# Optimization experiments

Hardware: AMD Instinct MI355X
Metric: run time of the kernel (lower is better)

Reference implementation:

```python
import jax, jax.numpy as jnp
import numpy as np

EMBED, HEADS, LEVELS, POINTS = 256, 8, 4, 4
SPATIAL_SHAPES = np.array([[128, 128], [64, 64], [32, 32], [16, 16]], dtype=np.int32)


def _grid_init_bias():
    # Faithful reproduction of the sampling_offsets bias init (per-head directional grid).
    thetas = np.arange(HEADS, dtype=np.float32) * (2.0 * np.pi / HEADS)
    g = np.stack([np.cos(thetas), np.sin(thetas)], -1)
    g = g / np.abs(g).max(-1, keepdims=True)
    g = np.tile(g.reshape(HEADS, 1, 1, 2), (1, LEVELS, POINTS, 1))
    for i in range(POINTS):
        g[:, :, i, :] *= i + 1
    return g.reshape(-1).astype(np.float32)


def setup_inputs() -> dict:
    key = jax.random.key(0)
    ks = jax.random.split(key, 8)
    bs = 2
    V = int((SPATIAL_SHAPES[:, 0] * SPATIAL_SHAPES[:, 1]).sum())  # 21760
    Q = V  # encoder self-attention
    C = EMBED
    n_off = HEADS * LEVELS * POINTS * 2
    n_attn = HEADS * LEVELS * POINTS
    inv_sqrt_c = 1.0 / np.sqrt(C)
    return {
        "query": jax.random.normal(ks[0], (bs, Q, C), jnp.float32),
        "value": jax.random.normal(ks[1], (bs, V, C), jnp.float32),
        "reference_points": jax.random.uniform(ks[2], (bs, Q, LEVELS, 2), jnp.float32),
        "spatial_shapes": SPATIAL_SHAPES,  # static int array
        # learned parameters (torch Linear stored as [in, out]: y = x @ W + b)
        "W_off": jax.random.normal(ks[3], (C, n_off), jnp.float32) * 0.01,
        "b_off": jnp.asarray(_grid_init_bias()),
        "W_attn": jax.random.normal(ks[4], (C, n_attn), jnp.float32) * 0.02,
        "b_attn": jnp.zeros((n_attn,), jnp.float32),
        "W_v": jax.random.normal(ks[5], (C, C), jnp.float32) * inv_sqrt_c,
        "b_v": jnp.zeros((C,), jnp.float32),
        "W_out": jax.random.normal(ks[6], (C, C), jnp.float32) * inv_sqrt_c,
        "b_out": jnp.zeros((C,), jnp.float32),
    }


def _ms_deform_attn(query, value, reference_points, shapes,
                    W_off, b_off, W_attn, b_attn, W_v, b_v, W_out, b_out):
    bs, Q, C = query.shape
    d = C // HEADS
    # value projection -> [bs, heads, V, d]
    val = (value @ W_v + b_v).reshape(bs, -1, HEADS, d).transpose(0, 2, 1, 3)
    # sampling offsets and attention weights from query
    off = (query @ W_off + b_off).reshape(bs, Q, HEADS, LEVELS, POINTS, 2)
    attn = jax.nn.softmax(
        (query @ W_attn + b_attn).reshape(bs, Q, HEADS, LEVELS * POINTS), axis=-1
    ).reshape(bs, Q, HEADS, LEVELS, POINTS)
    # offset normalizer is (W, H) per level
    norm = jnp.asarray(np.stack([shapes[:, 1], shapes[:, 0]], -1), jnp.float32)  # [L,2]
    loc = reference_points[:, :, None, :, None, :] + off / norm[None, None, None, :, None, :]

    out = jnp.zeros((bs, HEADS, Q, d), query.dtype)
    start = 0
    for l in range(LEVELS):
        H, W = int(shapes[l, 0]), int(shapes[l, 1])
        v_l = val[:, :, start:start + H * W]  # [bs, heads, H*W, d]
        start += H * W
        loc_l = loc[:, :, :, l]    # [bs, Q, heads, P, 2] in [0,1]
        attn_l = attn[:, :, :, l]  # [bs, Q, heads, P]
        # grid_sample(align_corners=False, padding_mode='zeros') semantics
        g = 2.0 * loc_l - 1.0
        x = (g[..., 0] + 1.0) * 0.5 * W - 0.5
        y = (g[..., 1] + 1.0) * 0.5 * H - 0.5
        x0 = jnp.floor(x)
        y0 = jnp.floor(y)
        for dx in (0, 1):
            for dy in (0, 1):
                xi = x0 + dx
                yi = y0 + dy
                w = (1.0 - jnp.abs(x - xi)) * (1.0 - jnp.abs(y - yi))
                valid = (xi >= 0) & (xi <= W - 1) & (yi >= 0) & (yi <= H - 1)
                w = jnp.where(valid, w, 0.0) * attn_l  # fused corner + attention weight
                idx = (jnp.clip(yi, 0, H - 1).astype(jnp.int32) * W
                       + jnp.clip(xi, 0, W - 1).astype(jnp.int32))  # [bs,Q,heads,P]
                idx_t = jnp.transpose(idx, (0, 2, 1, 3)).reshape(bs, HEADS, Q * POINTS)
                vals = jnp.take_along_axis(v_l, idx_t[..., None], axis=2)
                vals = vals.reshape(bs, HEADS, Q, POINTS, d)
                out = out + jnp.einsum('bhqpd,bqhp->bhqd', vals, w)
    out = out.transpose(0, 2, 1, 3).reshape(bs, Q, C)  # heads-major channel layout
    return out @ W_out + b_out


def reference(query, value, reference_points, spatial_shapes,
              W_off, b_off, W_attn, b_attn, W_v, b_v, W_out, b_out):
    shapes = np.asarray(spatial_shapes)  # static
    return _ms_deform_attn(query, value, reference_points, shapes,
                           W_off, b_off, W_attn, b_attn, W_v, b_v, W_out, b_out)
```

## Files before the change

kernel.cpp:

```cpp
#include <hip/hip_runtime.h>
#include <math.h>

#define QN 21760
#define MTOT 43520
#define SZBQC 11141120

typedef __attribute__((ext_vector_type(8))) short bf16x8;
typedef __attribute__((ext_vector_type(4))) float f32x4;
typedef __attribute__((ext_vector_type(2))) float f32x2;

__device__ inline ushort f2bf(float f) {
  union { float f; uint u; } v; v.f = f;
  return (ushort)((v.u + 0x7FFFu + ((v.u >> 16) & 1u)) >> 16);
}
__device__ inline float bflo(uint u) { union { uint u; float f; } v; v.u = u << 16; return v.f; }
__device__ inline float bfhi(uint u) { union { uint u; float f; } v; v.u = u & 0xFFFF0000u; return v.f; }
__device__ inline uint pk2(float lo, float hi) { return (uint)f2bf(lo) | ((uint)f2bf(hi) << 16); }

__device__ inline void g2l(const ushort* g, ushort* l) {
  __builtin_amdgcn_global_load_lds(
      (const __attribute__((address_space(1))) void*)g,
      (__attribute__((address_space(3))) void*)l, 16, 0, 0);
}

__global__ __launch_bounds__(256) void prep_weights(
    const float* __restrict__ Wv, const float* __restrict__ Wout,
    const float* __restrict__ Woff, const float* __restrict__ Wattn,
    const float* __restrict__ boff, const float* __restrict__ battn,
    ushort* __restrict__ wv_t, ushort* __restrict__ wout_t,
    ushort* __restrict__ wol_t, float* __restrict__ biasf) {
  int bidx = blockIdx.x, t = threadIdx.x;
  if (bidx < 256) {
    int idx = bidx * 256 + t; int n = idx >> 8, k = idx & 255;
    wv_t[idx] = f2bf(Wv[(size_t)k * 256 + n]);
  } else if (bidx < 512) {
    int idx = (bidx - 256) * 256 + t; int n = idx >> 8, k = idx & 255;
    wout_t[idx] = f2bf(Wout[(size_t)k * 256 + n]);
  } else {
    int idx = (bidx - 512) * 256 + t; int n = idx >> 8, k = idx & 255;
    float v = (n < 256) ? Woff[(size_t)k * 256 + n] : Wattn[(size_t)k * 128 + (n - 256)];
    wol_t[idx] = f2bf(v);
    if (idx < 384) biasf[idx] = (idx < 256) ? boff[idx] : battn[idx - 256];
  }
}

__global__ __launch_bounds__(256) void cast2_bf16(
    const float* __restrict__ q, const float* __restrict__ v,
    ushort* __restrict__ qo, ushort* __restrict__ vo) {
  int i = blockIdx.x * 256 + threadIdx.x;
  const float* src; ushort* dst;
  if (i >= SZBQC / 8) { src = q; dst = qo; i -= SZBQC / 8; }
  else { src = v; dst = vo; }
  const float4* xp = (const float4*)src;
  float4 a = xp[2 * i], b = xp[2 * i + 1];
  uint4 o;
  o.x = pk2(a.x, a.y); o.y = pk2(a.z, a.w);
  o.z = pk2(b.x, b.y); o.w = pk2(b.z, b.w);
  ((uint4*)dst)[i] = o;
}


__global__ __launch_bounds__(256) void gemm_in(
    const ushort* __restrict__ vbf, const ushort* __restrict__ qbf,
    const ushort* __restrict__ Wv, const ushort* __restrict__ Wol,
    const float* __restrict__ bv, const float* __restrict__ bol,
    ushort* __restrict__ val_out, float* __restrict__ offlog) {
  __shared__ ushort As[2][4096];
  __shared__ ushort Bs[2][4096];
  const int t = threadIdx.x, wave = t >> 6, lane = t & 63;
  const int bx = blockIdx.x, bm = blockIdx.y * 128;
  const bool isVal = bx < 2;
  const ushort* A  = isVal ? vbf : qbf;
  const ushort* Bt = isVal ? (Wv + (size_t)bx * 128 * 256)
                           : (Wol + (size_t)(bx - 2) * 128 * 256);
  const int wm = (wave >> 1) * 64, wn = (wave & 1) * 64;
  const int l15 = lane & 15, l4 = lane >> 4;
  const int pc = l4 ^ ((l15 >> 1) & 3);

  const int srow = lane >> 2;
  const int sch  = (lane & 3) ^ ((lane >> 3) & 3);
  const ushort* Ag = A + (size_t)(bm + 32 * wave + srow) * 256 + sch * 8;
  const ushort* Bg = Bt + (size_t)(32 * wave + srow) * 256 + sch * 8;
  ushort* la[2] = { &As[0][(32 * wave) * 32], &As[1][(32 * wave) * 32] };
  ushort* lb[2] = { &Bs[0][(32 * wave) * 32], &Bs[1][(32 * wave) * 32] };

  f32x4 acc[4][4];
#pragma unroll
  for (int i = 0; i < 4; ++i)
#pragma unroll
    for (int j = 0; j < 4; ++j) acc[i][j] = (f32x4){0.f, 0.f, 0.f, 0.f};

  g2l(Ag, la[0]); g2l(Ag + 16 * 256, la[0] + 16 * 32);
  g2l(Bg, lb[0]); g2l(Bg + 16 * 256, lb[0] + 16 * 32);

  for (int k = 0; k < 8; ++k) {
    __syncthreads();
    const int cur = k & 1, nxt = cur ^ 1;
    if (k < 7) {
      int k1 = (k + 1) * 32;
      g2l(Ag + k1, la[nxt]); g2l(Ag + 16 * 256 + k1, la[nxt] + 16 * 32);
      g2l(Bg + k1, lb[nxt]); g2l(Bg + 16 * 256 + k1, lb[nxt] + 16 * 32);
    }
    bf16x8 af[4], bfr[4];
#pragma unroll
    for (int mi = 0; mi < 4; ++mi)
      af[mi] = *(const bf16x8*)&As[cur][(wm + mi * 16 + l15) * 32 + pc * 8];
#pragma unroll
    for (int ni = 0; ni < 4; ++ni)
      bfr[ni] = *(const bf16x8*)&Bs[cur][(wn + ni * 16 + l15) * 32 + pc * 8];
#pragma unroll
    for (int mi = 0; mi < 4; ++mi)
#pragma unroll
      for (int ni = 0; ni < 4; ++ni)
        acc[mi][ni] = __builtin_amdgcn_mfma_f32_16x16x32_bf16(af[mi], bfr[ni], acc[mi][ni], 0, 0, 0);
  }

  if (isVal) {
#pragma unroll
    for (int mi = 0; mi < 4; ++mi)
#pragma unroll
      for (int ni = 0; ni < 4; ++ni) {
        int col = bx * 128 + wn + ni * 16 + l15;
        float bb = bv[col];
        int hh = col >> 5, c = col & 31;
#pragma unroll
        for (int r = 0; r < 4; ++r) {
          int row = bm + wm + mi * 16 + l4 * 4 + r;
          int b = (row >= QN) ? 1 : 0;
          int vpos = row - b * QN;
          val_out[((size_t)(b * 8 + hh) * QN + vpos) * 32 + c] = f2bf(acc[mi][ni][r] + bb);
        }
      }
  } else {
#pragma unroll
    for (int mi = 0; mi < 4; ++mi)
#pragma unroll
      for (int ni = 0; ni < 4; ++ni) {
        int col = (bx - 2) * 128 + wn + ni * 16 + l15;
        float bb = bol[col];
#pragma unroll
        for (int r = 0; r < 4; ++r) {
          int row = bm + wm + mi * 16 + l4 * 4 + r;
          offlog[(size_t)row * 384 + col] = acc[mi][ni][r] + bb;
        }
      }
  }
}

__global__ __launch_bounds__(256) void gemm_out(
    const ushort* __restrict__ A, const ushort* __restrict__ Bt,
    const float* __restrict__ bias, float* __restrict__ C) {
  __shared__ ushort As[2][4096];
  __shared__ ushort Bs[2][4096];
  const int t = threadIdx.x, wave = t >> 6, lane = t & 63;
  const int bm = blockIdx.y * 128, bn = blockIdx.x * 128;
  const int wm = (wave >> 1) * 64, wn = (wave & 1) * 64;
  const int l15 = lane & 15, l4 = lane >> 4;
  const int pc = l4 ^ ((l15 >> 1) & 3);

  const int srow = lane >> 2;
  const int sch  = (lane & 3) ^ ((lane >> 3) & 3);
  const ushort* Ag = A + (size_t)(bm + 32 * wave + srow) * 256 + sch * 8;
  const ushort* Bg = Bt + (size_t)(bn + 32 * wave + srow) * 256 + sch * 8;
  ushort* la[2] = { &As[0][(32 * wave) * 32], &As[1][(32 * wave) * 32] };
  ushort* lb[2] = { &Bs[0][(32 * wave) * 32], &Bs[1][(32 * wave) * 32] };

  f32x4 acc[4][4];
#pragma unroll
  for (int i = 0; i < 4; ++i)
#pragma unroll
    for (int j = 0; j < 4; ++j) acc[i][j] = (f32x4){0.f, 0.f, 0.f, 0.f};

  g2l(Ag, la[0]); g2l(Ag + 16 * 256, la[0] + 16 * 32);
  g2l(Bg, lb[0]); g2l(Bg + 16 * 256, lb[0] + 16 * 32);

  for (int k = 0; k < 8; ++k) {
    __syncthreads();
    const int cur = k & 1, nxt = cur ^ 1;
    if (k < 7) {
      int k1 = (k + 1) * 32;
      g2l(Ag + k1, la[nxt]); g2l(Ag + 16 * 256 + k1, la[nxt] + 16 * 32);
      g2l(Bg + k1, lb[nxt]); g2l(Bg + 16 * 256 + k1, lb[nxt] + 16 * 32);
    }
    bf16x8 af[4], bfr[4];
#pragma unroll
    for (int mi = 0; mi < 4; ++mi)
      af[mi] = *(const bf16x8*)&As[cur][(wm + mi * 16 + l15) * 32 + pc * 8];
#pragma unroll
    for (int ni = 0; ni < 4; ++ni)
      bfr[ni] = *(const bf16x8*)&Bs[cur][(wn + ni * 16 + l15) * 32 + pc * 8];
#pragma unroll
    for (int mi = 0; mi < 4; ++mi)
#pragma unroll
      for (int ni = 0; ni < 4; ++ni)
        acc[mi][ni] = __builtin_amdgcn_mfma_f32_16x16x32_bf16(af[mi], bfr[ni], acc[mi][ni], 0, 0, 0);
  }

#pragma unroll
  for (int mi = 0; mi < 4; ++mi)
#pragma unroll
    for (int ni = 0; ni < 4; ++ni) {
      int col = bn + wn + ni * 16 + l15;
      float bb = bias[col];
#pragma unroll
      for (int r = 0; r < 4; ++r) {
        int row = bm + wm + mi * 16 + l4 * 4 + r;
        C[(size_t)row * 256 + col] = acc[mi][ni][r] + bb;
      }
    }
}

__device__ inline void fma8(f32x2* a, uint4 u, float wv) {
  f32x2 ww = { wv, wv }; f32x2 v;
  v.x = bflo(u.x); v.y = bfhi(u.x); a[0] += v * ww;
  v.x = bflo(u.y); v.y = bfhi(u.y); a[1] += v * ww;
  v.x = bflo(u.z); v.y = bfhi(u.z); a[2] += v * ww;
  v.x = bflo(u.w); v.y = bfhi(u.w); a[3] += v * ww;
}

__global__ __launch_bounds__(256) void msda_sample(
    const ushort* __restrict__ val, const float* __restrict__ offlog,
    const float* __restrict__ ref, ushort* __restrict__ interm) {
  const int lsz[4]    = {128, 64, 32, 16};
  const int lstart[4] = {0, 16384, 20480, 21504};

  int h   = blockIdx.x & 7;
  int z   = blockIdx.x >> 3;
  int sub = threadIdx.x & 3;
  int bq  = z * 64 + (threadIdx.x >> 2);
  int b   = (bq >= QN) ? 1 : 0;

  const float* lgp = offlog + (size_t)bq * 384 + 256 + h * 16;
  float w[16];
  {
    float4 a0 = *(const float4*)(lgp);
    float4 a1 = *(const float4*)(lgp + 4);
    float4 a2 = *(const float4*)(lgp + 8);
    float4 a3 = *(const float4*)(lgp + 12);
    w[0]=a0.x; w[1]=a0.y; w[2]=a0.z; w[3]=a0.w;
    w[4]=a1.x; w[5]=a1.y; w[6]=a1.z; w[7]=a1.w;
    w[8]=a2.x; w[9]=a2.y; w[10]=a2.z; w[11]=a2.w;
    w[12]=a3.x; w[13]=a3.y; w[14]=a3.z; w[15]=a3.w;
  }
  float m = -1e30f;
#pragma unroll
  for (int s = 0; s < 16; ++s) m = fmaxf(m, w[s]);
  float sum = 0.f;
#pragma unroll
  for (int s = 0; s < 16; ++s) { w[s] = __expf(w[s] - m); sum += w[s]; }
  float inv = 1.f / sum;

  const float* offp = offlog + (size_t)bq * 384 + h * 32;
  const float* refp = ref + (size_t)bq * 8;
  const ushort* vb  = val + ((size_t)(b * 8 + h) * QN) * 32 + sub * 8;

  f32x2 acc[4];
#pragma unroll
  for (int i = 0; i < 4; ++i) acc[i] = (f32x2){0.f, 0.f};

#pragma unroll
  for (int l = 0; l < 4; ++l) {
    float4 o0 = *(const float4*)(offp + l * 8);
    float4 o1 = *(const float4*)(offp + l * 8 + 4);
    float ox[4] = { o0.x, o0.z, o1.x, o1.z };
    float oy[4] = { o0.y, o0.w, o1.y, o1.w };
    const int   W = lsz[l];
    const float fW = (float)W;
    const int   base = lstart[l];
    const float rx = refp[l * 2 + 0], ry = refp[l * 2 + 1];
#pragma unroll
    for (int p = 0; p < 4; ++p) {
      float x = rx * fW + ox[p] - 0.5f;
      float y = ry * fW + oy[p] - 0.5f;
      float x0f = floorf(x), y0f = floorf(y);
      int   x0 = (int)x0f,   y0 = (int)y0f;
      float fx = x - x0f,    fy = y - y0f;
      float a = w[l * 4 + p] * inv;
      const ushort* r0 = vb + (size_t)(base + y0 * W + x0) * 32;
      const ushort* r1 = r0 + (size_t)W * 32;

      if (x0 >= 0 && y0 >= 0 && x0 + 1 < W && y0 + 1 < W) {
        uint4 u00 = *(const uint4*)r0;
        uint4 u10 = *(const uint4*)(r0 + 32);
        uint4 u01 = *(const uint4*)r1;
        uint4 u11 = *(const uint4*)(r1 + 32);
        float w00 = (1.f - fx) * (1.f - fy) * a;
        float w10 = fx * (1.f - fy) * a;
        float w01 = (1.f - fx) * fy * a;
        float w11 = fx * fy * a;
        fma8(acc, u00, w00); fma8(acc, u10, w10);
        fma8(acc, u01, w01); fma8(acc, u11, w11);
      } else {
        float wx0 = (x0 >= 0 && x0 < W) ? (1.f - fx) : 0.f;
        float wx1 = (x0 + 1 >= 0 && x0 + 1 < W) ? fx : 0.f;
        float wy0 = (y0 >= 0 && y0 < W) ? (1.f - fy) : 0.f;
        float wy1 = (y0 + 1 >= 0 && y0 + 1 < W) ? fy : 0.f;
        float w00 = wx0 * wy0 * a, w10 = wx1 * wy0 * a;
        float w01 = wx0 * wy1 * a, w11 = wx1 * wy1 * a;
        if (w00 != 0.f) { uint4 u = *(const uint4*)r0;        fma8(acc, u, w00); }
        if (w10 != 0.f) { uint4 u = *(const uint4*)(r0 + 32); fma8(acc, u, w10); }
        if (w01 != 0.f) { uint4 u = *(const uint4*)r1;        fma8(acc, u, w01); }
        if (w11 != 0.f) { uint4 u = *(const uint4*)(r1 + 32); fma8(acc, u, w11); }
      }
    }
  }

  uint4 o;
  o.x = pk2(acc[0].x, acc[0].y); o.y = pk2(acc[1].x, acc[1].y);
  o.z = pk2(acc[2].x, acc[2].y); o.w = pk2(acc[3].x, acc[3].y);
  *(uint4*)(interm + (size_t)bq * 256 + h * 32 + sub * 8) = o;
}

extern "C" void kernel_launch(void* const* d_in, const int* in_sizes, int n_in,
                              void* d_out, int out_size, void* d_ws, size_t ws_size,
                              hipStream_t stream) {
  const float* query = (const float*)d_in[0];
  const float* value = (const float*)d_in[1];
  const float* ref   = (const float*)d_in[2];
  const float* W_off  = (const float*)d_in[4];
  const float* b_off  = (const float*)d_in[5];
  const float* W_attn = (const float*)d_in[6];
  const float* b_attn = (const float*)d_in[7];
  const float* W_v    = (const float*)d_in[8];
  const float* b_v    = (const float*)d_in[9];
  const float* W_out  = (const float*)d_in[10];
  const float* b_out  = (const float*)d_in[11];
  float* out = (float*)d_out;

  char* wsb = (char*)d_ws;
  ushort* ws_wv     = (ushort*)(wsb + 0);
  ushort* ws_wol    = (ushort*)(wsb + 131072);
  ushort* ws_wout   = (ushort*)(wsb + 327680);
  float*  ws_biasf  = (float*)(wsb + 458752);
  ushort* ws_val    = (ushort*)(wsb + 462848);
  ushort* ws_v      = (ushort*)(wsb + 22745088);
  ushort* ws_q      = (ushort*)(wsb + 45027328);
  ushort* ws_interm = ws_q;
  float*  ws_offlog = (float*)(wsb + 67309568);
  size_t need = (size_t)67309568 + 66846720;
  if (ws_size < need) return;

  dim3 blk(256);
  prep_weights<<<dim3(896), blk, 0, stream>>>(W_v, W_out, W_off, W_attn, b_off, b_attn,
                                              ws_wv, ws_wout, ws_wol, ws_biasf);
  cast2_bf16<<<dim3(2 * SZBQC / 8 / 256), blk, 0, stream>>>(query, value, ws_q, ws_v);
  gemm_in<<<dim3(5, 340), blk, 0, stream>>>(ws_v, ws_q, ws_wv, ws_wol, b_v, ws_biasf,
                                            ws_val, ws_offlog);
  msda_sample<<<dim3(5440), blk, 0, stream>>>(ws_val, ws_offlog, ref, ws_interm);
  gemm_out<<<dim3(2, 340), blk, 0, stream>>>(ws_interm, ws_wout, b_out, out);
}
```

Baseline: 303.4 us.

## Fuse fp32-to-bf16 cast into input GEMM and store values as fp16

Removes the separate cast kernel: gemm_in now loads fp32 query/value rows directly, converts them to bf16 in registers and writes the swizzled tile to LDS, overlapping the next-tile global loads with MFMA work. The projected value tensor is stored as fp16 and the sampler converts with native half-to-float casts instead of bf16 bit shifts. Grid dimensions are swapped so M tiles vary along x. This trades an extra full-tensor write/read pass for re-reading fp32 inputs once per N-block, and adds register-staged loads that may reduce load/compute overlap.

```diff
diff --git a/kernel.cpp b/kernel.cpp
--- a/kernel.cpp
+++ b/kernel.cpp
@@ -7,14 +7,11 @@
 
 typedef __attribute__((ext_vector_type(8))) short bf16x8;
 typedef __attribute__((ext_vector_type(4))) float f32x4;
-typedef __attribute__((ext_vector_type(2))) float f32x2;
 
 __device__ inline ushort f2bf(float f) {
   union { float f; uint u; } v; v.f = f;
   return (ushort)((v.u + 0x7FFFu + ((v.u >> 16) & 1u)) >> 16);
 }
-__device__ inline float bflo(uint u) { union { uint u; float f; } v; v.u = u << 16; return v.f; }
-__device__ inline float bfhi(uint u) { union { uint u; float f; } v; v.u = u & 0xFFFF0000u; return v.f; }
 __device__ inline uint pk2(float lo, float hi) { return (uint)f2bf(lo) | ((uint)f2bf(hi) << 16); }
 
 __device__ inline void g2l(const ushort* g, ushort* l) {
@@ -44,33 +41,18 @@
   }
 }
 
-__global__ __launch_bounds__(256) void cast2_bf16(
-    const float* __restrict__ q, const float* __restrict__ v,
-    ushort* __restrict__ qo, ushort* __restrict__ vo) {
-  int i = blockIdx.x * 256 + threadIdx.x;
-  const float* src; ushort* dst;
-  if (i >= SZBQC / 8) { src = q; dst = qo; i -= SZBQC / 8; }
-  else { src = v; dst = vo; }
-  const float4* xp = (const float4*)src;
-  float4 a = xp[2 * i], b = xp[2 * i + 1];
-  uint4 o;
-  o.x = pk2(a.x, a.y); o.y = pk2(a.z, a.w);
-  o.z = pk2(b.x, b.y); o.w = pk2(b.z, b.w);
-  ((uint4*)dst)[i] = o;
-}
-
 
 __global__ __launch_bounds__(256) void gemm_in(
-    const ushort* __restrict__ vbf, const ushort* __restrict__ qbf,
+    const float* __restrict__ value, const float* __restrict__ query,
     const ushort* __restrict__ Wv, const ushort* __restrict__ Wol,
     const float* __restrict__ bv, const float* __restrict__ bol,
     ushort* __restrict__ val_out, float* __restrict__ offlog) {
   __shared__ ushort As[2][4096];
   __shared__ ushort Bs[2][4096];
   const int t = threadIdx.x, wave = t >> 6, lane = t & 63;
-  const int bx = blockIdx.x, bm = blockIdx.y * 128;
+  const int bx = blockIdx.y, bm = blockIdx.x * 128;
   const bool isVal = bx < 2;
-  const ushort* A  = isVal ? vbf : qbf;
+  const float* A   = isVal ? value : query;
   const ushort* Bt = isVal ? (Wv + (size_t)bx * 128 * 256)
                            : (Wol + (size_t)(bx - 2) * 128 * 256);
   const int wm = (wave >> 1) * 64, wn = (wave & 1) * 64;
@@ -79,8 +61,116 @@
 
   const int srow = lane >> 2;
   const int sch  = (lane & 3) ^ ((lane >> 3) & 3);
+  const ushort* Bg = Bt + (size_t)(32 * wave + srow) * 256 + sch * 8;
+  ushort* lb[2] = { &Bs[0][(32 * wave) * 32], &Bs[1][(32 * wave) * 32] };
+
+  f32x4 acc[4][4];
+#pragma unroll
+  for (int i = 0; i < 4; ++i)
+#pragma unroll
+    for (int j = 0; j < 4; ++j) acc[i][j] = (f32x4){0.f, 0.f, 0.f, 0.f};
+
+  int arow[4], apart[4];
+#pragma unroll
+  for (int i = 0; i < 4; ++i) {
+    int c = t + i * 256; arow[i] = c >> 3; apart[i] = c & 7;
+  }
+
+  {
+    float4 pa[4];
+#pragma unroll
+    for (int i = 0; i < 4; ++i)
+      pa[i] = *(const float4*)&A[(size_t)(bm + arow[i]) * 256 + apart[i] * 4];
+    g2l(Bg, lb[0]); g2l(Bg + 16 * 256, lb[0] + 16 * 32);
+#pragma unroll
+    for (int i = 0; i < 4; ++i) {
+      int pc16 = (apart[i] >> 1) ^ ((arow[i] >> 1) & 3);
+      ushort4 hv = { f2bf(pa[i].x), f2bf(pa[i].y), f2bf(pa[i].z), f2bf(pa[i].w) };
+      *(ushort4*)&As[0][arow[i] * 32 + pc16 * 8 + (apart[i] & 1) * 4] = hv;
+    }
+  }
+
+  for (int k = 0; k < 8; ++k) {
+    __syncthreads();
+    const int cur = k & 1, nxt = cur ^ 1;
+    float4 pa[4];
+    if (k < 7) {
+      int k1 = (k + 1) * 32;
+#pragma unroll
+      for (int i = 0; i < 4; ++i)
+        pa[i] = *(const float4*)&A[(size_t)(bm + arow[i]) * 256 + k1 + apart[i] * 4];
+      g2l(Bg + k1, lb[nxt]); g2l(Bg + 16 * 256 + k1, lb[nxt] + 16 * 32);
+    }
+    bf16x8 af[4], bfr[4];
+#pragma unroll
+    for (int mi = 0; mi < 4; ++mi)
+      af[mi] = *(const bf16x8*)&As[cur][(wm + mi * 16 + l15) * 32 + pc * 8];
+#pragma unroll
+    for (int ni = 0; ni < 4; ++ni)
+      bfr[ni] = *(const bf16x8*)&Bs[cur][(wn + ni * 16 + l15) * 32 + pc * 8];
+#pragma unroll
+    for (int mi = 0; mi < 4; ++mi)
+#pragma unroll
+      for (int ni = 0; ni < 4; ++ni)
+        acc[mi][ni] = __builtin_amdgcn_mfma_f32_16x16x32_bf16(af[mi], bfr[ni], acc[mi][ni], 0, 0, 0);
+    if (k < 7) {
+#pragma unroll
+      for (int i = 0; i < 4; ++i) {
+        int pc16 = (apart[i] >> 1) ^ ((arow[i] >> 1) & 3);
+        ushort4 hv = { f2bf(pa[i].x), f2bf(pa[i].y), f2bf(pa[i].z), f2bf(pa[i].w) };
+        *(ushort4*)&As[nxt][arow[i] * 32 + pc16 * 8 + (apart[i] & 1) * 4] = hv;
+      }
+    }
+  }
+
+  if (isVal) {
+    _Float16* vo = (_Float16*)val_out;
+#pragma unroll
+    for (int mi = 0; mi < 4; ++mi)
+#pragma unroll
+      for (int ni = 0; ni < 4; ++ni) {
+        int col = bx * 128 + wn + ni * 16 + l15;
+        float bb = bv[col];
+        int hh = col >> 5, c = col & 31;
+#pragma unroll
+        for (int r = 0; r < 4; ++r) {
+          int row = bm + wm + mi * 16 + l4 * 4 + r;
+          int b = (row >= QN) ? 1 : 0;
+          int vpos = row - b * QN;
+          vo[((size_t)(b * 8 + hh) * QN + vpos) * 32 + c] = (_Float16)(acc[mi][ni][r] + bb);
+        }
+      }
+  } else {
+#pragma unroll
+    for (int mi = 0; mi < 4; ++mi)
+#pragma unroll
+      for (int ni = 0; ni < 4; ++ni) {
+        int col = (bx - 2) * 128 + wn + ni * 16 + l15;
+        float bb = bol[col];
+#pragma unroll
+        for (int r = 0; r < 4; ++r) {
+          int row = bm + wm + mi * 16 + l4 * 4 + r;
+          offlog[(size_t)row * 384 + col] = acc[mi][ni][r] + bb;
+        }
+      }
+  }
+}
+
+__global__ __launch_bounds__(256) void gemm_out(
+    const ushort* __restrict__ A, const ushort* __restrict__ Bt,
+    const float* __restrict__ bias, float* __restrict__ C) {
+  __shared__ ushort As[2][4096];
+  __shared__ ushort Bs[2][4096];
+  const int t = threadIdx.x, wave = t >> 6, lane = t & 63;
+  const int bm = blockIdx.x * 128, bn = blockIdx.y * 128;
+  const int wm = (wave >> 1) * 64, wn = (wave & 1) * 64;
+  const int l15 = lane & 15, l4 = lane >> 4;
+  const int pc = l4 ^ ((l15 >> 1) & 3);
+
+  const int srow = lane >> 2;
+  const int sch  = (lane & 3) ^ ((lane >> 3) & 3);
   const ushort* Ag = A + (size_t)(bm + 32 * wave + srow) * 256 + sch * 8;
-  const ushort* Bg = Bt + (size_t)(32 * wave + srow) * 256 + sch * 8;
+  const ushort* Bg = Bt + (size_t)(bn + 32 * wave + srow) * 256 + sch * 8;
   ushort* la[2] = { &As[0][(32 * wave) * 32], &As[1][(32 * wave) * 32] };
   ushort* lb[2] = { &Bs[0][(32 * wave) * 32], &Bs[1][(32 * wave) * 32] };
 
@@ -115,87 +205,6 @@
         acc[mi][ni] = __builtin_amdgcn_mfma_f32_16x16x32_bf16(af[mi], bfr[ni], acc[mi][ni], 0, 0, 0);
   }
 
-  if (isVal) {
-#pragma unroll
-    for (int mi = 0; mi < 4; ++mi)
-#pragma unroll
-      for (int ni = 0; ni < 4; ++ni) {
-        int col = bx * 128 + wn + ni * 16 + l15;
-        float bb = bv[col];
-        int hh = col >> 5, c = col & 31;
-#pragma unroll
-        for (int r = 0; r < 4; ++r) {
-          int row = bm + wm + mi * 16 + l4 * 4 + r;
-          int b = (row >= QN) ? 1 : 0;
-          int vpos = row - b * QN;
-          val_out[((size_t)(b * 8 + hh) * QN + vpos) * 32 + c] = f2bf(acc[mi][ni][r] + bb);
-        }
-      }
-  } else {
-#pragma unroll
-    for (int mi = 0; mi < 4; ++mi)
-#pragma unroll
-      for (int ni = 0; ni < 4; ++ni) {
-        int col = (bx - 2) * 128 + wn + ni * 16 + l15;
-        float bb = bol[col];
-#pragma unroll
-        for (int r = 0; r < 4; ++r) {
-          int row = bm + wm + mi * 16 + l4 * 4 + r;
-          offlog[(size_t)row * 384 + col] = acc[mi][ni][r] + bb;
-        }
-      }
-  }
-}
-
-__global__ __launch_bounds__(256) void gemm_out(
-    const ushort* __restrict__ A, const ushort* __restrict__ Bt,
-    const float* __restrict__ bias, float* __restrict__ C) {
-  __shared__ ushort As[2][4096];
-  __shared__ ushort Bs[2][4096];
-  const int t = threadIdx.x, wave = t >> 6, lane = t & 63;
-  const int bm = blockIdx.y * 128, bn = blockIdx.x * 128;
-  const int wm = (wave >> 1) * 64, wn = (wave & 1) * 64;
-  const int l15 = lane & 15, l4 = lane >> 4;
-  const int pc = l4 ^ ((l15 >> 1) & 3);
-
-  const int srow = lane >> 2;
-  const int sch  = (lane & 3) ^ ((lane >> 3) & 3);
-  const ushort* Ag = A + (size_t)(bm + 32 * wave + srow) * 256 + sch * 8;
-  const ushort* Bg = Bt + (size_t)(bn + 32 * wave + srow) * 256 + sch * 8;
-  ushort* la[2] = { &As[0][(32 * wave) * 32], &As[1][(32 * wave) * 32] };
-  ushort* lb[2] = { &Bs[0][(32 * wave) * 32], &Bs[1][(32 * wave) * 32] };
-
-  f32x4 acc[4][4];
-#pragma unroll
-  for (int i = 0; i < 4; ++i)
-#pragma unroll
-    for (int j = 0; j < 4; ++j) acc[i][j] = (f32x4){0.f, 0.f, 0.f, 0.f};
-
-  g2l(Ag, la[0]); g2l(Ag + 16 * 256, la[0] + 16 * 32);
-  g2l(Bg, lb[0]); g2l(Bg + 16 * 256, lb[0] + 16 * 32);
-
-  for (int k = 0; k < 8; ++k) {
-    __syncthreads();
-    const int cur = k & 1, nxt = cur ^ 1;
-    if (k < 7) {
-      int k1 = (k + 1) * 32;
-      g2l(Ag + k1, la[nxt]); g2l(Ag + 16 * 256 + k1, la[nxt] + 16 * 32);
-      g2l(Bg + k1, lb[nxt]); g2l(Bg + 16 * 256 + k1, lb[nxt] + 16 * 32);
-    }
-    bf16x8 af[4], bfr[4];
-#pragma unroll
-    for (int mi = 0; mi < 4; ++mi)
-      af[mi] = *(const bf16x8*)&As[cur][(wm + mi * 16 + l15) * 32 + pc * 8];
-#pragma unroll
-    for (int ni = 0; ni < 4; ++ni)
-      bfr[ni] = *(const bf16x8*)&Bs[cur][(wn + ni * 16 + l15) * 32 + pc * 8];
-#pragma unroll
-    for (int mi = 0; mi < 4; ++mi)
-#pragma unroll
-      for (int ni = 0; ni < 4; ++ni)
-        acc[mi][ni] = __builtin_amdgcn_mfma_f32_16x16x32_bf16(af[mi], bfr[ni], acc[mi][ni], 0, 0, 0);
-  }
-
 #pragma unroll
   for (int mi = 0; mi < 4; ++mi)
 #pragma unroll
@@ -210,12 +219,10 @@
     }
 }
 
-__device__ inline void fma8(f32x2* a, uint4 u, float wv) {
-  f32x2 ww = { wv, wv }; f32x2 v;
-  v.x = bflo(u.x); v.y = bfhi(u.x); a[0] += v * ww;
-  v.x = bflo(u.y); v.y = bfhi(u.y); a[1] += v * ww;
-  v.x = bflo(u.z); v.y = bfhi(u.z); a[2] += v * ww;
-  v.x = bflo(u.w); v.y = bfhi(u.w); a[3] += v * ww;
+__device__ inline void fmah(float* a, uint4 u, float wv) {
+  union { uint4 u; _Float16 h[8]; } c; c.u = u;
+#pragma unroll
+  for (int i = 0; i < 8; ++i) a[i] = fmaf((float)c.h[i], wv, a[i]);
 }
 
 __global__ __launch_bounds__(256) void msda_sample(
@@ -254,9 +261,9 @@
   const float* refp = ref + (size_t)bq * 8;
   const ushort* vb  = val + ((size_t)(b * 8 + h) * QN) * 32 + sub * 8;
 
-  f32x2 acc[4];
-#pragma unroll
-  for (int i = 0; i < 4; ++i) acc[i] = (f32x2){0.f, 0.f};
+  float acc[8];
+#pragma unroll
+  for (int i = 0; i < 8; ++i) acc[i] = 0.f;
 
 #pragma unroll
   for (int l = 0; l < 4; ++l) {
@@ -288,8 +295,8 @@
         float w10 = fx * (1.f - fy) * a;
         float w01 = (1.f - fx) * fy * a;
         float w11 = fx * fy * a;
-        fma8(acc, u00, w00); fma8(acc, u10, w10);
-        fma8(acc, u01, w01); fma8(acc, u11, w11);
+        fmah(acc, u00, w00); fmah(acc, u10, w10);
+        fmah(acc, u01, w01); fmah(acc, u11, w11);
       } else {
         float wx0 = (x0 >= 0 && x0 < W) ? (1.f - fx) : 0.f;
         float wx1 = (x0 + 1 >= 0 && x0 + 1 < W) ? fx : 0.f;
@@ -297,17 +304,17 @@
         float wy1 = (y0 + 1 >= 0 && y0 + 1 < W) ? fy : 0.f;
         float w00 = wx0 * wy0 * a, w10 = wx1 * wy0 * a;
         float w01 = wx0 * wy1 * a, w11 = wx1 * wy1 * a;
-        if (w00 != 0.f) { uint4 u = *(const uint4*)r0;        fma8(acc, u, w00); }
-        if (w10 != 0.f) { uint4 u = *(const uint4*)(r0 + 32); fma8(acc, u, w10); }
-        if (w01 != 0.f) { uint4 u = *(const uint4*)r1;        fma8(acc, u, w01); }
-        if (w11 != 0.f) { uint4 u = *(const uint4*)(r1 + 32); fma8(acc, u, w11); }
+        if (w00 != 0.f) { uint4 u = *(const uint4*)r0;        fmah(acc, u, w00); }
+        if (w10 != 0.f) { uint4 u = *(const uint4*)(r0 + 32); fmah(acc, u, w10); }
+        if (w01 != 0.f) { uint4 u = *(const uint4*)r1;        fmah(acc, u, w01); }
+        if (w11 != 0.f) { uint4 u = *(const uint4*)(r1 + 32); fmah(acc, u, w11); }
       }
     }
   }
 
   uint4 o;
-  o.x = pk2(acc[0].x, acc[0].y); o.y = pk2(acc[1].x, acc[1].y);
-  o.z = pk2(acc[2].x, acc[2].y); o.w = pk2(acc[3].x, acc[3].y);
+  o.x = pk2(acc[0], acc[1]); o.y = pk2(acc[2], acc[3]);
+  o.z = pk2(acc[4], acc[5]); o.w = pk2(acc[6], acc[7]);
   *(uint4*)(interm + (size_t)bq * 256 + h * 32 + sub * 8) = o;
 }
 
@@ -333,19 +340,16 @@
   ushort* ws_wout   = (ushort*)(wsb + 327680);
   float*  ws_biasf  = (float*)(wsb + 458752);
   ushort* ws_val    = (ushort*)(wsb + 462848);
-  ushort* ws_v      = (ushort*)(wsb + 22745088);
-  ushort* ws_q      = (ushort*)(wsb + 45027328);
-  ushort* ws_interm = ws_q;
-  float*  ws_offlog = (float*)(wsb + 67309568);
-  size_t need = (size_t)67309568 + 66846720;
+  ushort* ws_interm = (ushort*)(wsb + 22745088);
+  float*  ws_offlog = (float*)(wsb + 45027328);
+  size_t need = (size_t)45027328 + 66846720;
   if (ws_size < need) return;
 
   dim3 blk(256);
   prep_weights<<<dim3(896), blk, 0, stream>>>(W_v, W_out, W_off, W_attn, b_off, b_attn,
                                               ws_wv, ws_wout, ws_wol, ws_biasf);
-  cast2_bf16<<<dim3(2 * SZBQC / 8 / 256), blk, 0, stream>>>(query, value, ws_q, ws_v);
-  gemm_in<<<dim3(5, 340), blk, 0, stream>>>(ws_v, ws_q, ws_wv, ws_wol, b_v, ws_biasf,
+  gemm_in<<<dim3(340, 5), blk, 0, stream>>>(value, query, ws_wv, ws_wol, b_v, ws_biasf,
                                             ws_val, ws_offlog);
   msda_sample<<<dim3(5440), blk, 0, stream>>>(ws_val, ws_offlog, ref, ws_interm);
-  gemm_out<<<dim3(2, 340), blk, 0, stream>>>(ws_interm, ws_wout, b_out, out);
-}
+  gemm_out<<<dim3(340, 2), blk, 0, stream>>>(ws_interm, ws_wout, b_out, out);
+}
```

Result: faster. 286.6 us (-5.5%).
